# Kernel optimization log

Measured on AMD Instinct MI355X. Metric: run time of the kernel, lower is better.

The kernel has to match this reference:

```python
import jax, jax.numpy as jnp
import numpy as np

B, S, H = 4, 8192, 768
NH, HD = 12, 64          # num_heads, head_size
M = 64                   # projection_dim = min(256, HD)
EPS = 1e-6

def setup_inputs() -> dict:
    key = jax.random.key(0)
    ks = jax.random.split(key, 10)
    scale_w = 0.02
    scale_p = 1.0 / np.sqrt(HD)
    return {
        'hidden_states': jax.random.normal(ks[0], (B, S, H), jnp.float32),
        'Wq': jax.random.normal(ks[1], (H, H), jnp.float32) * scale_w,
        'bq': jnp.zeros((H,), jnp.float32),
        'Wk': jax.random.normal(ks[2], (H, H), jnp.float32) * scale_w,
        'bk': jnp.zeros((H,), jnp.float32),
        'Wv': jax.random.normal(ks[3], (H, H), jnp.float32) * scale_w,
        'bv': jnp.zeros((H,), jnp.float32),
        'Wo': jax.random.normal(ks[4], (H, H), jnp.float32) * scale_w,
        'bo': jnp.zeros((H,), jnp.float32),
        'projection_matrix': jax.random.normal(ks[5], (NH, HD, M), jnp.float32) * scale_p,
    }

def reference(hidden_states, Wq, bq, Wk, bk, Wv, bv, Wo, bo, projection_matrix):
    b, s, h = hidden_states.shape
    def heads(x):  # [b,s,h] -> [b,nh,s,hd]
        return x.reshape(b, s, NH, HD).transpose(0, 2, 1, 3)
    q = heads(hidden_states @ Wq + bq)
    k = heads(hidden_states @ Wk + bk)
    v = heads(hidden_states @ Wv + bv)
    # random-feature projection + stabilized exp feature map
    qp = jnp.einsum('bhnd,hdm->bhnm', q, projection_matrix)
    kp = jnp.einsum('bhnd,hdm->bhnm', k, projection_matrix)
    qp = jnp.exp(qp - jnp.max(qp, axis=-1, keepdims=True))
    kp = jnp.exp(kp - jnp.max(kp, axis=-1, keepdims=True))
    # O(n) linear attention: kv summary [b,h,m,hd]
    kv = jnp.einsum('bhnm,bhnd->bhmd', kp, v)
    qkv = jnp.einsum('bhnm,bhmd->bhnd', qp, kv)
    k_sum = jnp.sum(kp, axis=2)                      # [b,h,m]
    normalizer = jnp.einsum('bhnm,bhm->bhn', qp, k_sum)[..., None]
    ctx = qkv / (normalizer + EPS)
    ctx = ctx.transpose(0, 2, 1, 3).reshape(b, s, NH * HD)
    return ctx @ Wo + bo
```

## Files before the change

kernel.cpp:

```cpp
#include <hip/hip_runtime.h>
#include <hip/hip_bf16.h>


#define S_    8192
#define H_    768
#define NH_   12
#define EPS_  1e-6f

typedef unsigned short U16;
typedef short bf16x8 __attribute__((ext_vector_type(8)));
typedef float f32x4  __attribute__((ext_vector_type(4)));

__device__ __forceinline__ U16 f2b(float x) {
  unsigned u = __float_as_uint(x);
  return (U16)((u + 0x7fffu + ((u >> 16) & 1u)) >> 16);
}
__device__ __forceinline__ float b2f(U16 h) {
  return __uint_as_float(((unsigned)h) << 16);
}
__device__ __forceinline__ void gl2lds16(const void* g, void* l) {
  __builtin_amdgcn_global_load_lds(
      (const __attribute__((address_space(1))) void*)g,
      (__attribute__((address_space(3))) void*)l, 16, 0, 0);
}

__global__ void zero_f32(float* __restrict__ p, int n) {
  int i = blockIdx.x * 256 + threadIdx.x;
  if (i < n) p[i] = 0.f;
}

__global__ void cvt_f32_bf16(const float* __restrict__ src, U16* __restrict__ hi, int n4) {
  int i = blockIdx.x * 256 + threadIdx.x;
  if (i >= n4) return;
  float4 x = ((const float4*)src)[i];
  ushort4 h;
  h.x = f2b(x.x); h.y = f2b(x.y); h.z = f2b(x.z); h.w = f2b(x.w);
  ((ushort4*)hi)[i] = h;
}

__global__ void fold_proj(const float* __restrict__ Wq, const float* __restrict__ bq,
                          const float* __restrict__ Wk, const float* __restrict__ bk,
                          const float* __restrict__ P,
                          float* __restrict__ Wqp, float* __restrict__ bqp,
                          float* __restrict__ Wkp, float* __restrict__ bkp) {
  __shared__ float Pl[64 * 64];
  __shared__ float WL[4 * 64];
  int h = blockIdx.y, kc = blockIdx.x, tid = threadIdx.x;
  const float* W  = blockIdx.z ? Wk : Wq;
  const float* bb = blockIdx.z ? bk : bq;
  float* Wout = blockIdx.z ? Wkp : Wqp;
  float* bout = blockIdx.z ? bkp : bqp;
  const float4* P4 = (const float4*)(P + (size_t)h * 4096);
#pragma unroll
  for (int i = 0; i < 4; ++i) ((float4*)Pl)[tid + i * 256] = P4[tid + i * 256];
  WL[tid] = W[(size_t)(kc * 4 + (tid >> 6)) * H_ + h * 64 + (tid & 63)];
  __syncthreads();
  int kl = tid >> 6, m = tid & 63;
  float acc = 0.f;
#pragma unroll
  for (int d = 0; d < 64; ++d) acc += WL[kl * 64 + d] * Pl[d * 64 + m];
  Wout[(size_t)(kc * 4 + kl) * H_ + h * 64 + m] = acc;
  if (kc == 0 && tid < 64) {
    float a2 = 0.f;
    for (int d = 0; d < 64; ++d) a2 += bb[h * 64 + d] * Pl[d * 64 + tid];
    bout[h * 64 + tid] = a2;
  }
}

__global__ void build_cat(const float* __restrict__ Wqp, const float* __restrict__ Wkp,
                          const float* __restrict__ Wv,  const float* __restrict__ Wo,
                          U16* __restrict__ WcatH, U16* __restrict__ WoTH) {
  int k = blockIdx.x * 256 + threadIdx.x;
  int r = blockIdx.y;
  float v; U16* dh; size_t off;
  if (r < 768)       { v = Wqp[(size_t)k * H_ + r];          off = (size_t)r * H_ + k;          dh = WcatH; }
  else if (r < 1536) { v = Wkp[(size_t)k * H_ + (r - 768)];  off = (size_t)r * H_ + k;          dh = WcatH; }
  else if (r < 2304) { v = Wv [(size_t)k * H_ + (r - 1536)]; off = (size_t)r * H_ + k;          dh = WcatH; }
  else               { v = Wo [(size_t)k * H_ + (r - 2304)]; off = (size_t)(r - 2304) * H_ + k; dh = WoTH; }
  dh[off] = f2b(v);
}

__global__ void build_bias(const float* __restrict__ bqp, const float* __restrict__ bkp,
                           const float* __restrict__ bv, float* __restrict__ biasC) {
  int i = blockIdx.x * 256 + threadIdx.x;
  if (i >= 2304) return;
  biasC[i] = i < 768 ? bqp[i] : (i < 1536 ? bkp[i - 768] : bv[i - 1536]);
}

#define GEMM_KLOOP()                                                         \
  auto stage = [&](int kt, int bi) {                                         \
    const U16* ap = As + kt * 64;                                            \
    const U16* bp = Bs + kt * 64;                                            \
    unsigned ub = (unsigned)bi * 32768u + lb;                                \
    _Pragma("unroll")                                                        \
    for (int q = 0; q < 4; ++q) {                                            \
      gl2lds16(ap + (size_t)(q * 64) * H_, &Us[ub + q * 4096]);              \
      gl2lds16(bp + (size_t)(q * 64) * H_, &Us[ub + 16384u + q * 4096]);     \
    }                                                                        \
  };                                                                         \
  auto swzo = [&](int ks) { return (((ks * 4 + quad) ^ (l16 & 7)) * 8); };   \
  stage(0, 0);                                                               \
  for (int t = 0; t < 12; ++t) {                                             \
    const unsigned ab = (unsigned)(t & 1) * 32768u;                          \
    if (t < 11) {                                                            \
      stage(t + 1, (t + 1) & 1);                                             \
      asm volatile("s_waitcnt vmcnt(8)" ::: "memory");                       \
    } else {                                                                 \
      asm volatile("s_waitcnt vmcnt(0)" ::: "memory");                       \
    }                                                                        \
    __builtin_amdgcn_sched_barrier(0);                                       \
    __builtin_amdgcn_s_barrier();                                            \
    __builtin_amdgcn_sched_barrier(0);                                       \
    bf16x8 ah[8], bh[4];                                                     \
                              \
    _Pragma("unroll")                                                        \
    for (int i = 0; i < 4; ++i)                                              \
      _Pragma("unroll")                                                      \
      for (int ks = 0; ks < 2; ++ks)                                         \
        ah[i * 2 + ks] = *(const bf16x8*)&Us[ab +                            \
            (unsigned)((wm * 128 + i * 16 + l16) * 64 + swzo(ks))];          \
    _Pragma("unroll")                                                        \
    for (int jj = 0; jj < 2; ++jj)                                           \
      _Pragma("unroll")                                                      \
      for (int ks = 0; ks < 2; ++ks)                                         \
        bh[jj * 2 + ks] = *(const bf16x8*)&Us[ab + 16384u +                  \
            (unsigned)((wn * 64 + jj * 16 + l16) * 64 + swzo(ks))];          \
    PHASE_TAIL(0, 0)                                                         \
                                          \
    _Pragma("unroll")                                                        \
    for (int jj = 0; jj < 2; ++jj)                                           \
      _Pragma("unroll")                                                      \
      for (int ks = 0; ks < 2; ++ks)                                         \
        bh[jj * 2 + ks] = *(const bf16x8*)&Us[ab + 16384u +                  \
            (unsigned)((wn * 64 + (2 + jj) * 16 + l16) * 64 + swzo(ks))];    \
    PHASE_TAIL(0, 1)                                                         \
                              \
    _Pragma("unroll")                                                        \
    for (int i = 0; i < 4; ++i)                                              \
      _Pragma("unroll")                                                      \
      for (int ks = 0; ks < 2; ++ks)                                         \
        ah[i * 2 + ks] = *(const bf16x8*)&Us[ab +                            \
            (unsigned)((wm * 128 + 64 + i * 16 + l16) * 64 + swzo(ks))];     \
    PHASE_TAIL(1, 1)                                                         \
                              \
    _Pragma("unroll")                                                        \
    for (int jj = 0; jj < 2; ++jj)                                           \
      _Pragma("unroll")                                                      \
      for (int ks = 0; ks < 2; ++ks)                                         \
        bh[jj * 2 + ks] = *(const bf16x8*)&Us[ab + 16384u +                  \
            (unsigned)((wn * 64 + jj * 16 + l16) * 64 + swzo(ks))];          \
    PHASE_TAIL(1, 0)                                                         \
  }

#define PHASE_TAIL(mh, jh)                                                   \
    __builtin_amdgcn_sched_barrier(0);                                       \
    __builtin_amdgcn_s_barrier();                                            \
    asm volatile("s_waitcnt lgkmcnt(0)" ::: "memory");                       \
    __builtin_amdgcn_sched_barrier(0);                                       \
    __builtin_amdgcn_s_setprio(1);                                           \
    _Pragma("unroll")                                                        \
    for (int jj = 0; jj < 2; ++jj)                                           \
      _Pragma("unroll")                                                      \
      for (int i = 0; i < 4; ++i)                                            \
        _Pragma("unroll")                                                    \
        for (int ks = 0; ks < 2; ++ks)                                       \
          acc[(mh) * 4 + i][(jh) * 2 + jj] =                                 \
              __builtin_amdgcn_mfma_f32_16x16x32_bf16(                       \
                  ah[i * 2 + ks], bh[jj * 2 + ks],                           \
                  acc[(mh) * 4 + i][(jh) * 2 + jj], 0, 0, 0);                \
    __builtin_amdgcn_s_setprio(0);                                           \
    __builtin_amdgcn_sched_barrier(0);                                       \
    __builtin_amdgcn_s_barrier();                                            \
    __builtin_amdgcn_sched_barrier(0);

__global__ __launch_bounds__(512, 2) void gemm_qkv(
    const U16* __restrict__ Ahi, const U16* __restrict__ Bhi,
    const float* __restrict__ bias,
    U16* __restrict__ qp, U16* __restrict__ kpT, U16* __restrict__ vT) {
  __shared__ __align__(16) U16 Us[65536];
  const int tid = threadIdx.x, w = tid >> 6, lane = tid & 63;
  const int quad = lane >> 4, l16 = lane & 15;
  const int id = blockIdx.x;
  const int xcd = id & 7, pos = id >> 3;
  const int mt = xcd * 16 + pos / 9, nt = pos % 9;
  const int rowA0 = mt * 256, colB0 = nt * 256;
  const int wm = w >> 2, wn = w & 3;
  const int srow = w * 8 + (lane >> 3);
  const int kch = ((lane & 7) ^ (lane >> 3)) * 8;
  const U16* As = Ahi + (size_t)(rowA0 + srow) * H_ + kch;
  const U16* Bs = Bhi + (size_t)(colB0 + srow) * H_ + kch;
  const unsigned lb = (unsigned)(w * 8) * 64;

  f32x4 acc[8][4] = {};
  GEMM_KLOOP()

  const int col64 = colB0 + wn * 64;
  float bj[4];
#pragma unroll
  for (int j = 0; j < 4; ++j) bj[j] = bias[col64 + j * 16 + l16];
  if (col64 < 768) {
    const int h = col64 >> 6;
#pragma unroll
    for (int f = 0; f < 8; ++f) {
#pragma unroll
      for (int r = 0; r < 4; ++r) {
        int row = rowA0 + wm * 128 + f * 16 + quad * 4 + r;
        float v0 = acc[f][0][r] + bj[0], v1 = acc[f][1][r] + bj[1];
        float v2 = acc[f][2][r] + bj[2], v3 = acc[f][3][r] + bj[3];
        float mx = fmaxf(fmaxf(v0, v1), fmaxf(v2, v3));
        mx = fmaxf(mx, __shfl_xor(mx, 1));
        mx = fmaxf(mx, __shfl_xor(mx, 2));
        mx = fmaxf(mx, __shfl_xor(mx, 4));
        mx = fmaxf(mx, __shfl_xor(mx, 8));
        int b = row >> 13, s = row & 8191;
        size_t base = ((size_t)(b * NH_ + h) * S_ + s) * 64 + l16;
        qp[base +  0] = f2b(__expf(v0 - mx));
        qp[base + 16] = f2b(__expf(v1 - mx));
        qp[base + 32] = f2b(__expf(v2 - mx));
        qp[base + 48] = f2b(__expf(v3 - mx));
      }
    }
  } else {
    const int isv = col64 >= 1536;
    const int h = (col64 - (isv ? 1536 : 768)) >> 6;
    U16* dstT = isv ? vT : kpT;
#pragma unroll
    for (int f = 0; f < 8; ++f) {
      float er[4][4];
#pragma unroll
      for (int r = 0; r < 4; ++r) {
        float v0 = acc[f][0][r] + bj[0], v1 = acc[f][1][r] + bj[1];
        float v2 = acc[f][2][r] + bj[2], v3 = acc[f][3][r] + bj[3];
        if (!isv) {
          float mx = fmaxf(fmaxf(v0, v1), fmaxf(v2, v3));
          mx = fmaxf(mx, __shfl_xor(mx, 1));
          mx = fmaxf(mx, __shfl_xor(mx, 2));
          mx = fmaxf(mx, __shfl_xor(mx, 4));
          mx = fmaxf(mx, __shfl_xor(mx, 8));
          v0 = __expf(v0 - mx); v1 = __expf(v1 - mx);
          v2 = __expf(v2 - mx); v3 = __expf(v3 - mx);
        }
        er[0][r] = v0; er[1][r] = v1; er[2][r] = v2; er[3][r] = v3;
      }
      int n = rowA0 + wm * 128 + f * 16 + quad * 4;
      int b = n >> 13, s = n & 8191;
      int bh2 = b * NH_ + h;
#pragma unroll
      for (int j = 0; j < 4; ++j) {
        ushort4 o;
        o.x = f2b(er[j][0]); o.y = f2b(er[j][1]);
        o.z = f2b(er[j][2]); o.w = f2b(er[j][3]);
        *(ushort4*)&dstT[((size_t)bh2 * 64 + j * 16 + l16) * S_ + s] = o;
      }
    }
  }
}

__global__ __launch_bounds__(256, 4) void kv_accum_mfma(
    const U16* __restrict__ kpT, const U16* __restrict__ vT,
    float* __restrict__ kvT) {
  __shared__ __align__(16) U16 Us[2 * 64 * 64];
  const int tid = threadIdx.x, w = tid >> 6, lane = tid & 63;
  const int quad = lane >> 4, l16 = lane & 15;
  const int bh = blockIdx.y;
  const int n0 = blockIdx.x * 512;
  const U16* srcs[4];
  unsigned ldsoff[4];
#pragma unroll
  for (int t = 0; t < 4; ++t) {
    int c = w * 4 + t, buf = c >> 3;
    int r = (c & 7) * 8 + (lane >> 3);
    const U16* base = buf ? kpT : vT;
    srcs[t] = base + ((size_t)bh * 64 + r) * S_ + n0 + (lane & 7) * 8;
    ldsoff[t] = buf * 4096 + (c & 7) * 512;
  }
  f32x4 acc[4] = {};
  float ks[4] = {0.f, 0.f, 0.f, 0.f};
  for (int nc = 0; nc < 512; nc += 64) {
#pragma unroll
    for (int t = 0; t < 4; ++t) gl2lds16(srcs[t] + nc, &Us[ldsoff[t]]);
    __syncthreads();
#pragma unroll
    for (int k0 = 0; k0 < 64; k0 += 32) {
      bf16x8 av = *(const bf16x8*)&Us[(w * 16 + l16) * 64 + k0 + quad * 8];
#pragma unroll
      for (int j = 0; j < 4; ++j) {
        bf16x8 bk = *(const bf16x8*)&Us[4096 + (j * 16 + l16) * 64 + k0 + quad * 8];
        if (w == 0) {
#pragma unroll
          for (int e = 0; e < 8; ++e) ks[j] += b2f((U16)bk[e]);
        }
        acc[j] = __builtin_amdgcn_mfma_f32_16x16x32_bf16(av, bk, acc[j], 0, 0, 0);
      }
    }
    __syncthreads();
  }
#pragma unroll
  for (int j = 0; j < 4; ++j)
#pragma unroll
    for (int r = 0; r < 4; ++r) {
      int d = w * 16 + quad * 4 + r;
      atomicAdd(&kvT[((size_t)bh * 80 + d) * 64 + j * 16 + l16], acc[j][r]);
    }
  if (w == 0) {
#pragma unroll
    for (int j = 0; j < 4; ++j) {
      ks[j] += __shfl_xor(ks[j], 16);
      ks[j] += __shfl_xor(ks[j], 32);
    }
    if (lane < 16) {
#pragma unroll
      for (int j = 0; j < 4; ++j)
        atomicAdd(&kvT[((size_t)bh * 80 + 64) * 64 + j * 16 + lane], ks[j]);
    }
  }
}

__global__ __launch_bounds__(256) void ctx_gemm_k(
    const U16* __restrict__ qp, const float* __restrict__ kvT,
    U16* __restrict__ ctx) {
  __shared__ __align__(16) U16 As[128 * 64];
  __shared__ __align__(16) U16 Bs[80 * 64];
  int bh = blockIdx.y, row0 = blockIdx.x * 128;
  int tid = threadIdx.x, w = tid >> 6, lane = tid & 63;
  int quad = lane >> 4, l16 = lane & 15;
  const U16* Ab = qp + ((size_t)bh * S_ + row0) * 64;
#pragma unroll
  for (int t = 0; t < 4; ++t) {
    int cb = (w * 4 + t) * 64;
    gl2lds16(Ab + (size_t)(cb + lane) * 8, &As[cb * 8]);
  }
  const float4* kv4 = (const float4*)(kvT + (size_t)bh * 5120);
#pragma unroll
  for (int t = 0; t < 5; ++t) {
    int idx = t * 256 + tid;
    float4 f = kv4[idx];
    ushort4 o;
    o.x = f2b(f.x); o.y = f2b(f.y); o.z = f2b(f.z); o.w = f2b(f.w);
    *(ushort4*)&Bs[idx * 4] = o;
  }
  __syncthreads();
  f32x4 acc[2][5] = {};
#pragma unroll
  for (int k0 = 0; k0 < 64; k0 += 32) {
    bf16x8 a[2], fb[5];
#pragma unroll
    for (int i = 0; i < 2; ++i)
      a[i] = *(const bf16x8*)&As[(w * 32 + i * 16 + l16) * 64 + k0 + quad * 8];
#pragma unroll
    for (int j = 0; j < 5; ++j)
      fb[j] = *(const bf16x8*)&Bs[(j * 16 + l16) * 64 + k0 + quad * 8];
#pragma unroll
    for (int j = 0; j < 5; ++j)
#pragma unroll
      for (int i = 0; i < 2; ++i)
        acc[i][j] = __builtin_amdgcn_mfma_f32_16x16x32_bf16(a[i], fb[j], acc[i][j], 0, 0, 0);
  }
  int b = bh / NH_, h = bh - b * NH_;
#pragma unroll
  for (int i = 0; i < 2; ++i) {
#pragma unroll
    for (int r = 0; r < 4; ++r) {
      int s = row0 + w * 32 + i * 16 + quad * 4 + r;
      float nv = __shfl(acc[i][4][r], lane & 48);
      float inv = 1.f / (nv + EPS_);
      size_t base = ((size_t)b * S_ + s) * H_ + h * 64;
#pragma unroll
      for (int j = 0; j < 4; ++j)
        ctx[base + j * 16 + l16] = f2b(acc[i][j][r] * inv);
    }
  }
}

__global__ __launch_bounds__(512, 2) void gemm_out(
    const U16* __restrict__ Ahi, const U16* __restrict__ Bhi,
    const float* __restrict__ bias, float* __restrict__ C) {
  __shared__ __align__(16) U16 Us[65536];
  const int tid = threadIdx.x, w = tid >> 6, lane = tid & 63;
  const int quad = lane >> 4, l16 = lane & 15;
  const int id = blockIdx.x;
  const int xcd = id & 7, pos = id >> 3;
  const int mt = xcd * 16 + pos / 3, nt = pos % 3;
  const int rowA0 = mt * 256, colB0 = nt * 256;
  const int wm = w >> 2, wn = w & 3;
  const int srow = w * 8 + (lane >> 3);
  const int kch = ((lane & 7) ^ (lane >> 3)) * 8;
  const U16* As = Ahi + (size_t)(rowA0 + srow) * H_ + kch;
  const U16* Bs = Bhi + (size_t)(colB0 + srow) * H_ + kch;
  const unsigned lb = (unsigned)(w * 8) * 64;

  f32x4 acc[8][4] = {};
  GEMM_KLOOP()

#pragma unroll
  for (int f = 0; f < 8; ++f) {
    int row = rowA0 + wm * 128 + f * 16 + quad * 4;
#pragma unroll
    for (int j = 0; j < 4; ++j) {
      int col = colB0 + wn * 64 + j * 16 + l16;
      float bvv = bias[col];
#pragma unroll
      for (int r = 0; r < 4; ++r)
        C[(size_t)(row + r) * H_ + col] = acc[f][j][r] + bvv;
    }
  }
}

extern "C" void kernel_launch(void* const* d_in, const int* in_sizes, int n_in,
                              void* d_out, int out_size, void* d_ws, size_t ws_size,
                              hipStream_t stream) {
  const float* hs = (const float*)d_in[0];
  const float* Wq = (const float*)d_in[1];
  const float* bq = (const float*)d_in[2];
  const float* Wk = (const float*)d_in[3];
  const float* bk = (const float*)d_in[4];
  const float* Wv = (const float*)d_in[5];
  const float* bv = (const float*)d_in[6];
  const float* Wo = (const float*)d_in[7];
  const float* bo = (const float*)d_in[8];
  const float* P  = (const float*)d_in[9];
  float* out = (float*)d_out;

  char* ws = (char*)d_ws;
  size_t off = 0;
  auto alloc = [&](size_t bytes) -> void* {
    void* p = ws + off;
    off = (off + bytes + 255) & ~(size_t)255;
    return p;
  };
  U16*   hs_hi = (U16*)alloc(50331648);
  float* WqpF  = (float*)alloc(2359296);
  float* WkpF  = (float*)alloc(2359296);
  float* bqpF  = (float*)alloc(3072);
  float* bkpF  = (float*)alloc(3072);
  U16*   WcatH = (U16*)alloc(3538944);
  U16*   WoTH  = (U16*)alloc(1179648);
  float* biasC = (float*)alloc(9216);
  U16*   qp    = (U16*)alloc(50331648);
  U16*   kpT   = (U16*)alloc(50331648);
  U16*   vT    = (U16*)alloc(50331648);
  float* kvT   = (float*)alloc(983040);
  U16*   ctx   = hs_hi;

  zero_f32<<<dim3(960), dim3(256), 0, stream>>>(kvT, 245760);
  cvt_f32_bf16<<<dim3(24576), dim3(256), 0, stream>>>(hs, hs_hi, 6291456);
  fold_proj<<<dim3(192, 12, 2), dim3(256), 0, stream>>>(Wq, bq, Wk, bk, P, WqpF, bqpF, WkpF, bkpF);
  build_cat<<<dim3(3, 3072), dim3(256), 0, stream>>>(WqpF, WkpF, Wv, Wo, WcatH, WoTH);
  build_bias<<<dim3(9), dim3(256), 0, stream>>>(bqpF, bkpF, bv, biasC);
  gemm_qkv<<<dim3(1152), dim3(512), 0, stream>>>(hs_hi, WcatH, biasC, qp, kpT, vT);
  kv_accum_mfma<<<dim3(16, 48), dim3(256), 0, stream>>>(kpT, vT, kvT);
  ctx_gemm_k<<<dim3(64, 48), dim3(256), 0, stream>>>(qp, kvT, ctx);
  gemm_out<<<dim3(384), dim3(512), 0, stream>>>(ctx, WoTH, bo, out);
}
```

Before: 496.2 us.

## Make QKV GEMM persistent over N tiles and tile-transpose weight conversion

The QKV projection GEMM changes from 1152 blocks of 512 threads using 256x256 tiles to 512 blocks of 256 threads using 128x128 tiles. Each block keeps one 128-row A tile and loops over 9 column tiles, prefetching the next tile's first K slice across tile boundaries. The weight transpose-and-convert kernel now goes through a padded shared-memory tile, so both reads and writes are coalesced and vectorised instead of strided per element. The smaller tiles lower arithmetic intensity per block and give fewer blocks for parallelism, in exchange for better A reuse in L2 and continuous pipelining across output tiles.

```diff
diff --git a/kernel.cpp b/kernel.cpp
--- a/kernel.cpp
+++ b/kernel.cpp
@@ -67,17 +67,32 @@
   }
 }
 
-__global__ void build_cat(const float* __restrict__ Wqp, const float* __restrict__ Wkp,
-                          const float* __restrict__ Wv,  const float* __restrict__ Wo,
-                          U16* __restrict__ WcatH, U16* __restrict__ WoTH) {
-  int k = blockIdx.x * 256 + threadIdx.x;
-  int r = blockIdx.y;
-  float v; U16* dh; size_t off;
-  if (r < 768)       { v = Wqp[(size_t)k * H_ + r];          off = (size_t)r * H_ + k;          dh = WcatH; }
-  else if (r < 1536) { v = Wkp[(size_t)k * H_ + (r - 768)];  off = (size_t)r * H_ + k;          dh = WcatH; }
-  else if (r < 2304) { v = Wv [(size_t)k * H_ + (r - 1536)]; off = (size_t)r * H_ + k;          dh = WcatH; }
-  else               { v = Wo [(size_t)k * H_ + (r - 2304)]; off = (size_t)(r - 2304) * H_ + k; dh = WoTH; }
-  dh[off] = f2b(v);
+__global__ void build_cat_t(const float* __restrict__ Wqp, const float* __restrict__ Wkp,
+                            const float* __restrict__ Wv,  const float* __restrict__ Wo,
+                            U16* __restrict__ WcatH, U16* __restrict__ WoTH) {
+  __shared__ float T[64][68];
+  const int kb = blockIdx.x, rb = blockIdx.y, mat = blockIdx.z;
+  const int tid = threadIdx.x;
+  const float* W = mat == 0 ? Wqp : (mat == 1 ? Wkp : (mat == 2 ? Wv : Wo));
+#pragma unroll
+  for (int p = 0; p < 4; ++p) {
+    int idx = tid + p * 256;
+    int rr = idx >> 4, c4 = (idx & 15) * 4;
+    float4 v = *(const float4*)&W[(size_t)(kb * 64 + rr) * H_ + rb * 64 + c4];
+    T[rr][c4] = v.x; T[rr][c4 + 1] = v.y; T[rr][c4 + 2] = v.z; T[rr][c4 + 3] = v.w;
+  }
+  __syncthreads();
+  U16* dst = mat == 3 ? WoTH : WcatH;
+  const int rbase = (mat == 3 ? 0 : mat * 768) + rb * 64;
+#pragma unroll
+  for (int p = 0; p < 4; ++p) {
+    int idx = tid + p * 256;
+    int r2 = idx >> 4, c2 = (idx & 15) * 4;
+    ushort4 o;
+    o.x = f2b(T[c2 + 0][r2]); o.y = f2b(T[c2 + 1][r2]);
+    o.z = f2b(T[c2 + 2][r2]); o.w = f2b(T[c2 + 3][r2]);
+    *(ushort4*)&dst[(size_t)(rbase + r2) * H_ + kb * 64 + c2] = o;
+  }
 }
 
 __global__ void build_bias(const float* __restrict__ bqp, const float* __restrict__ bkp,
@@ -85,6 +100,267 @@
   int i = blockIdx.x * 256 + threadIdx.x;
   if (i >= 2304) return;
   biasC[i] = i < 768 ? bqp[i] : (i < 1536 ? bkp[i - 768] : bv[i - 1536]);
+}
+
+__global__ __launch_bounds__(256, 2) void gemm_qkv(
+    const U16* __restrict__ Ahi, const U16* __restrict__ Bhi,
+    const float* __restrict__ bias,
+    U16* __restrict__ qp, U16* __restrict__ kpT, U16* __restrict__ vT) {
+  __shared__ __align__(16) U16 Us[32768];
+  const int tid = threadIdx.x, w = tid >> 6, lane = tid & 63;
+  const int quad = lane >> 4, l16 = lane & 15;
+  const int b = blockIdx.x;
+  const int mt = b & 255, nt0 = b >> 8;
+  const int rowA0 = mt * 128;
+  const int wm = w & 1, wn = w >> 1;
+  const U16* srcA[4];
+  int rowBl[4];
+  unsigned ldsc[4];
+  const int kch = ((lane & 7) ^ (lane >> 3)) * 8;
+#pragma unroll
+  for (int t = 0; t < 4; ++t) {
+    int c = w * 4 + t;
+    int row = c * 8 + (lane >> 3);
+    srcA[t] = Ahi + (size_t)(rowA0 + row) * H_ + kch;
+    rowBl[t] = row;
+    ldsc[t] = (unsigned)c * 512;
+  }
+  auto stage = [&](int jn, int tn, int bi) {
+    const int colB = (nt0 + 2 * jn) * 128;
+    unsigned ub = (unsigned)bi * 16384u;
+#pragma unroll
+    for (int t = 0; t < 4; ++t) {
+      gl2lds16(srcA[t] + tn * 64, &Us[ub + ldsc[t]]);
+      gl2lds16(Bhi + (size_t)(colB + rowBl[t]) * H_ + tn * 64 + kch,
+               &Us[ub + 8192u + ldsc[t]]);
+    }
+  };
+
+  stage(0, 0, 0);
+  for (int jj = 0; jj < 9; ++jj) {
+    const int colB0 = (nt0 + 2 * jj) * 128;
+    f32x4 acc[4][4] = {};
+    for (int t = 0; t < 12; ++t) {
+      const bool more = !(jj == 8 && t == 11);
+      if (more) {
+        if (t < 11) stage(jj, t + 1, (t + 1) & 1);
+        else        stage(jj + 1, 0, 0);
+        asm volatile("s_waitcnt vmcnt(8)" ::: "memory");
+      } else {
+        asm volatile("s_waitcnt vmcnt(0)" ::: "memory");
+      }
+      __builtin_amdgcn_sched_barrier(0);
+      __builtin_amdgcn_s_barrier();
+      __builtin_amdgcn_sched_barrier(0);
+      const unsigned ab = (unsigned)(t & 1) * 16384u;
+      bf16x8 ah[4][2], bh[4][2];
+#pragma unroll
+      for (int i = 0; i < 4; ++i)
+#pragma unroll
+        for (int ks = 0; ks < 2; ++ks)
+          ah[i][ks] = *(const bf16x8*)&Us[ab +
+              (unsigned)((wm * 64 + i * 16 + l16) * 64 +
+                         (((ks * 4 + quad) ^ (l16 & 7)) * 8))];
+#pragma unroll
+      for (int j = 0; j < 4; ++j)
+#pragma unroll
+        for (int ks = 0; ks < 2; ++ks)
+          bh[j][ks] = *(const bf16x8*)&Us[ab + 8192u +
+              (unsigned)((wn * 64 + j * 16 + l16) * 64 +
+                         (((ks * 4 + quad) ^ (l16 & 7)) * 8))];
+      asm volatile("s_waitcnt lgkmcnt(0)" ::: "memory");
+      __builtin_amdgcn_sched_barrier(0);
+      __builtin_amdgcn_s_setprio(1);
+#pragma unroll
+      for (int ks = 0; ks < 2; ++ks)
+#pragma unroll
+        for (int j = 0; j < 4; ++j)
+#pragma unroll
+          for (int i = 0; i < 4; ++i)
+            acc[i][j] = __builtin_amdgcn_mfma_f32_16x16x32_bf16(
+                ah[i][ks], bh[j][ks], acc[i][j], 0, 0, 0);
+      __builtin_amdgcn_s_setprio(0);
+      __builtin_amdgcn_sched_barrier(0);
+      __builtin_amdgcn_s_barrier();
+      __builtin_amdgcn_sched_barrier(0);
+    }
+    const int col64 = colB0 + wn * 64;
+    float bj[4];
+#pragma unroll
+    for (int j = 0; j < 4; ++j) bj[j] = bias[col64 + j * 16 + l16];
+    if (col64 < 768) {
+      const int h = col64 >> 6;
+#pragma unroll
+      for (int i = 0; i < 4; ++i) {
+#pragma unroll
+        for (int r = 0; r < 4; ++r) {
+          int row = rowA0 + wm * 64 + i * 16 + quad * 4 + r;
+          float v0 = acc[i][0][r] + bj[0], v1 = acc[i][1][r] + bj[1];
+          float v2 = acc[i][2][r] + bj[2], v3 = acc[i][3][r] + bj[3];
+          float mx = fmaxf(fmaxf(v0, v1), fmaxf(v2, v3));
+          mx = fmaxf(mx, __shfl_xor(mx, 1));
+          mx = fmaxf(mx, __shfl_xor(mx, 2));
+          mx = fmaxf(mx, __shfl_xor(mx, 4));
+          mx = fmaxf(mx, __shfl_xor(mx, 8));
+          int bb = row >> 13, s = row & 8191;
+          size_t base = ((size_t)(bb * NH_ + h) * S_ + s) * 64 + l16;
+          qp[base +  0] = f2b(__expf(v0 - mx));
+          qp[base + 16] = f2b(__expf(v1 - mx));
+          qp[base + 32] = f2b(__expf(v2 - mx));
+          qp[base + 48] = f2b(__expf(v3 - mx));
+        }
+      }
+    } else {
+      const int isv = col64 >= 1536;
+      const int h = (col64 - (isv ? 1536 : 768)) >> 6;
+      U16* dstT = isv ? vT : kpT;
+      const int bh2 = (rowA0 >> 13) * NH_ + h;
+#pragma unroll
+      for (int i = 0; i < 4; ++i) {
+        float er[4][4];
+#pragma unroll
+        for (int r = 0; r < 4; ++r) {
+          float v0 = acc[i][0][r] + bj[0], v1 = acc[i][1][r] + bj[1];
+          float v2 = acc[i][2][r] + bj[2], v3 = acc[i][3][r] + bj[3];
+          if (!isv) {
+            float mx = fmaxf(fmaxf(v0, v1), fmaxf(v2, v3));
+            mx = fmaxf(mx, __shfl_xor(mx, 1));
+            mx = fmaxf(mx, __shfl_xor(mx, 2));
+            mx = fmaxf(mx, __shfl_xor(mx, 4));
+            mx = fmaxf(mx, __shfl_xor(mx, 8));
+            v0 = __expf(v0 - mx); v1 = __expf(v1 - mx);
+            v2 = __expf(v2 - mx); v3 = __expf(v3 - mx);
+          }
+          er[0][r] = v0; er[1][r] = v1; er[2][r] = v2; er[3][r] = v3;
+        }
+        int n = rowA0 + wm * 64 + i * 16 + quad * 4;
+        int s = n & 8191;
+#pragma unroll
+        for (int j = 0; j < 4; ++j) {
+          ushort4 o;
+          o.x = f2b(er[j][0]); o.y = f2b(er[j][1]);
+          o.z = f2b(er[j][2]); o.w = f2b(er[j][3]);
+          *(ushort4*)&dstT[((size_t)bh2 * 64 + j * 16 + l16) * S_ + s] = o;
+        }
+      }
+    }
+  }
+}
+
+__global__ __launch_bounds__(256, 4) void kv_accum_mfma(
+    const U16* __restrict__ kpT, const U16* __restrict__ vT,
+    float* __restrict__ kvT) {
+  __shared__ __align__(16) U16 Us[2 * 64 * 64];
+  const int tid = threadIdx.x, w = tid >> 6, lane = tid & 63;
+  const int quad = lane >> 4, l16 = lane & 15;
+  const int bh = blockIdx.y;
+  const int n0 = blockIdx.x * 512;
+  const U16* srcs[4];
+  unsigned ldsoff[4];
+#pragma unroll
+  for (int t = 0; t < 4; ++t) {
+    int c = w * 4 + t, buf = c >> 3;
+    int r = (c & 7) * 8 + (lane >> 3);
+    const U16* base = buf ? kpT : vT;
+    srcs[t] = base + ((size_t)bh * 64 + r) * S_ + n0 + (lane & 7) * 8;
+    ldsoff[t] = buf * 4096 + (c & 7) * 512;
+  }
+  f32x4 acc[4] = {};
+  float ks[4] = {0.f, 0.f, 0.f, 0.f};
+  for (int nc = 0; nc < 512; nc += 64) {
+#pragma unroll
+    for (int t = 0; t < 4; ++t) gl2lds16(srcs[t] + nc, &Us[ldsoff[t]]);
+    __syncthreads();
+#pragma unroll
+    for (int k0 = 0; k0 < 64; k0 += 32) {
+      bf16x8 av = *(const bf16x8*)&Us[(w * 16 + l16) * 64 + k0 + quad * 8];
+#pragma unroll
+      for (int j = 0; j < 4; ++j) {
+        bf16x8 bk = *(const bf16x8*)&Us[4096 + (j * 16 + l16) * 64 + k0 + quad * 8];
+        if (w == 0) {
+#pragma unroll
+          for (int e = 0; e < 8; ++e) ks[j] += b2f((U16)bk[e]);
+        }
+        acc[j] = __builtin_amdgcn_mfma_f32_16x16x32_bf16(av, bk, acc[j], 0, 0, 0);
+      }
+    }
+    __syncthreads();
+  }
+#pragma unroll
+  for (int j = 0; j < 4; ++j)
+#pragma unroll
+    for (int r = 0; r < 4; ++r) {
+      int d = w * 16 + quad * 4 + r;
+      atomicAdd(&kvT[((size_t)bh * 80 + d) * 64 + j * 16 + l16], acc[j][r]);
+    }
+  if (w == 0) {
+#pragma unroll
+    for (int j = 0; j < 4; ++j) {
+      ks[j] += __shfl_xor(ks[j], 16);
+      ks[j] += __shfl_xor(ks[j], 32);
+    }
+    if (lane < 16) {
+#pragma unroll
+      for (int j = 0; j < 4; ++j)
+        atomicAdd(&kvT[((size_t)bh * 80 + 64) * 64 + j * 16 + lane], ks[j]);
+    }
+  }
+}
+
+__global__ __launch_bounds__(256) void ctx_gemm_k(
+    const U16* __restrict__ qp, const float* __restrict__ kvT,
+    U16* __restrict__ ctx) {
+  __shared__ __align__(16) U16 As[128 * 64];
+  __shared__ __align__(16) U16 Bs[80 * 64];
+  int bh = blockIdx.y, row0 = blockIdx.x * 128;
+  int tid = threadIdx.x, w = tid >> 6, lane = tid & 63;
+  int quad = lane >> 4, l16 = lane & 15;
+  const U16* Ab = qp + ((size_t)bh * S_ + row0) * 64;
+#pragma unroll
+  for (int t = 0; t < 4; ++t) {
+    int cb = (w * 4 + t) * 64;
+    gl2lds16(Ab + (size_t)(cb + lane) * 8, &As[cb * 8]);
+  }
+  const float4* kv4 = (const float4*)(kvT + (size_t)bh * 5120);
+#pragma unroll
+  for (int t = 0; t < 5; ++t) {
+    int idx = t * 256 + tid;
+    float4 f = kv4[idx];
+    ushort4 o;
+    o.x = f2b(f.x); o.y = f2b(f.y); o.z = f2b(f.z); o.w = f2b(f.w);
+    *(ushort4*)&Bs[idx * 4] = o;
+  }
+  __syncthreads();
+  f32x4 acc[2][5] = {};
+#pragma unroll
+  for (int k0 = 0; k0 < 64; k0 += 32) {
+    bf16x8 a[2], fb[5];
+#pragma unroll
+    for (int i = 0; i < 2; ++i)
+      a[i] = *(const bf16x8*)&As[(w * 32 + i * 16 + l16) * 64 + k0 + quad * 8];
+#pragma unroll
+    for (int j = 0; j < 5; ++j)
+      fb[j] = *(const bf16x8*)&Bs[(j * 16 + l16) * 64 + k0 + quad * 8];
+#pragma unroll
+    for (int j = 0; j < 5; ++j)
+#pragma unroll
+      for (int i = 0; i < 2; ++i)
+        acc[i][j] = __builtin_amdgcn_mfma_f32_16x16x32_bf16(a[i], fb[j], acc[i][j], 0, 0, 0);
+  }
+  int b = bh / NH_, h = bh - b * NH_;
+#pragma unroll
+  for (int i = 0; i < 2; ++i) {
+#pragma unroll
+    for (int r = 0; r < 4; ++r) {
+      int s = row0 + w * 32 + i * 16 + quad * 4 + r;
+      float nv = __shfl(acc[i][4][r], lane & 48);
+      float inv = 1.f / (nv + EPS_);
+      size_t base = ((size_t)b * S_ + s) * H_ + h * 64;
+#pragma unroll
+      for (int j = 0; j < 4; ++j)
+        ctx[base + j * 16 + l16] = f2b(acc[i][j][r] * inv);
+    }
+  }
 }
 
 #define GEMM_KLOOP()                                                         \
@@ -112,7 +388,6 @@
     __builtin_amdgcn_s_barrier();                                            \
     __builtin_amdgcn_sched_barrier(0);                                       \
     bf16x8 ah[8], bh[4];                                                     \
-                              \
     _Pragma("unroll")                                                        \
     for (int i = 0; i < 4; ++i)                                              \
       _Pragma("unroll")                                                      \
@@ -126,7 +401,6 @@
         bh[jj * 2 + ks] = *(const bf16x8*)&Us[ab + 16384u +                  \
             (unsigned)((wn * 64 + jj * 16 + l16) * 64 + swzo(ks))];          \
     PHASE_TAIL(0, 0)                                                         \
-                                          \
     _Pragma("unroll")                                                        \
     for (int jj = 0; jj < 2; ++jj)                                           \
       _Pragma("unroll")                                                      \
@@ -134,7 +408,6 @@
         bh[jj * 2 + ks] = *(const bf16x8*)&Us[ab + 16384u +                  \
             (unsigned)((wn * 64 + (2 + jj) * 16 + l16) * 64 + swzo(ks))];    \
     PHASE_TAIL(0, 1)                                                         \
-                              \
     _Pragma("unroll")                                                        \
     for (int i = 0; i < 4; ++i)                                              \
       _Pragma("unroll")                                                      \
@@ -142,7 +415,6 @@
         ah[i * 2 + ks] = *(const bf16x8*)&Us[ab +                            \
             (unsigned)((wm * 128 + 64 + i * 16 + l16) * 64 + swzo(ks))];     \
     PHASE_TAIL(1, 1)                                                         \
-                              \
     _Pragma("unroll")                                                        \
     for (int jj = 0; jj < 2; ++jj)                                           \
       _Pragma("unroll")                                                      \
@@ -172,205 +444,6 @@
     __builtin_amdgcn_sched_barrier(0);                                       \
     __builtin_amdgcn_s_barrier();                                            \
     __builtin_amdgcn_sched_barrier(0);
-
-__global__ __launch_bounds__(512, 2) void gemm_qkv(
-    const U16* __restrict__ Ahi, const U16* __restrict__ Bhi,
-    const float* __restrict__ bias,
-    U16* __restrict__ qp, U16* __restrict__ kpT, U16* __restrict__ vT) {
-  __shared__ __align__(16) U16 Us[65536];
-  const int tid = threadIdx.x, w = tid >> 6, lane = tid & 63;
-  const int quad = lane >> 4, l16 = lane & 15;
-  const int id = blockIdx.x;
-  const int xcd = id & 7, pos = id >> 3;
-  const int mt = xcd * 16 + pos / 9, nt = pos % 9;
-  const int rowA0 = mt * 256, colB0 = nt * 256;
-  const int wm = w >> 2, wn = w & 3;
-  const int srow = w * 8 + (lane >> 3);
-  const int kch = ((lane & 7) ^ (lane >> 3)) * 8;
-  const U16* As = Ahi + (size_t)(rowA0 + srow) * H_ + kch;
-  const U16* Bs = Bhi + (size_t)(colB0 + srow) * H_ + kch;
-  const unsigned lb = (unsigned)(w * 8) * 64;
-
-  f32x4 acc[8][4] = {};
-  GEMM_KLOOP()
-
-  const int col64 = colB0 + wn * 64;
-  float bj[4];
-#pragma unroll
-  for (int j = 0; j < 4; ++j) bj[j] = bias[col64 + j * 16 + l16];
-  if (col64 < 768) {
-    const int h = col64 >> 6;
-#pragma unroll
-    for (int f = 0; f < 8; ++f) {
-#pragma unroll
-      for (int r = 0; r < 4; ++r) {
-        int row = rowA0 + wm * 128 + f * 16 + quad * 4 + r;
-        float v0 = acc[f][0][r] + bj[0], v1 = acc[f][1][r] + bj[1];
-        float v2 = acc[f][2][r] + bj[2], v3 = acc[f][3][r] + bj[3];
-        float mx = fmaxf(fmaxf(v0, v1), fmaxf(v2, v3));
-        mx = fmaxf(mx, __shfl_xor(mx, 1));
-        mx = fmaxf(mx, __shfl_xor(mx, 2));
-        mx = fmaxf(mx, __shfl_xor(mx, 4));
-        mx = fmaxf(mx, __shfl_xor(mx, 8));
-        int b = row >> 13, s = row & 8191;
-        size_t base = ((size_t)(b * NH_ + h) * S_ + s) * 64 + l16;
-        qp[base +  0] = f2b(__expf(v0 - mx));
-        qp[base + 16] = f2b(__expf(v1 - mx));
-        qp[base + 32] = f2b(__expf(v2 - mx));
-        qp[base + 48] = f2b(__expf(v3 - mx));
-      }
-    }
-  } else {
-    const int isv = col64 >= 1536;
-    const int h = (col64 - (isv ? 1536 : 768)) >> 6;
-    U16* dstT = isv ? vT : kpT;
-#pragma unroll
-    for (int f = 0; f < 8; ++f) {
-      float er[4][4];
-#pragma unroll
-      for (int r = 0; r < 4; ++r) {
-        float v0 = acc[f][0][r] + bj[0], v1 = acc[f][1][r] + bj[1];
-        float v2 = acc[f][2][r] + bj[2], v3 = acc[f][3][r] + bj[3];
-        if (!isv) {
-          float mx = fmaxf(fmaxf(v0, v1), fmaxf(v2, v3));
-          mx = fmaxf(mx, __shfl_xor(mx, 1));
-          mx = fmaxf(mx, __shfl_xor(mx, 2));
-          mx = fmaxf(mx, __shfl_xor(mx, 4));
-          mx = fmaxf(mx, __shfl_xor(mx, 8));
-          v0 = __expf(v0 - mx); v1 = __expf(v1 - mx);
-          v2 = __expf(v2 - mx); v3 = __expf(v3 - mx);
-        }
-        er[0][r] = v0; er[1][r] = v1; er[2][r] = v2; er[3][r] = v3;
-      }
-      int n = rowA0 + wm * 128 + f * 16 + quad * 4;
-      int b = n >> 13, s = n & 8191;
-      int bh2 = b * NH_ + h;
-#pragma unroll
-      for (int j = 0; j < 4; ++j) {
-        ushort4 o;
-        o.x = f2b(er[j][0]); o.y = f2b(er[j][1]);
-        o.z = f2b(er[j][2]); o.w = f2b(er[j][3]);
-        *(ushort4*)&dstT[((size_t)bh2 * 64 + j * 16 + l16) * S_ + s] = o;
-      }
-    }
-  }
-}
-
-__global__ __launch_bounds__(256, 4) void kv_accum_mfma(
-    const U16* __restrict__ kpT, const U16* __restrict__ vT,
-    float* __restrict__ kvT) {
-  __shared__ __align__(16) U16 Us[2 * 64 * 64];
-  const int tid = threadIdx.x, w = tid >> 6, lane = tid & 63;
-  const int quad = lane >> 4, l16 = lane & 15;
-  const int bh = blockIdx.y;
-  const int n0 = blockIdx.x * 512;
-  const U16* srcs[4];
-  unsigned ldsoff[4];
-#pragma unroll
-  for (int t = 0; t < 4; ++t) {
-    int c = w * 4 + t, buf = c >> 3;
-    int r = (c & 7) * 8 + (lane >> 3);
-    const U16* base = buf ? kpT : vT;
-    srcs[t] = base + ((size_t)bh * 64 + r) * S_ + n0 + (lane & 7) * 8;
-    ldsoff[t] = buf * 4096 + (c & 7) * 512;
-  }
-  f32x4 acc[4] = {};
-  float ks[4] = {0.f, 0.f, 0.f, 0.f};
-  for (int nc = 0; nc < 512; nc += 64) {
-#pragma unroll
-    for (int t = 0; t < 4; ++t) gl2lds16(srcs[t] + nc, &Us[ldsoff[t]]);
-    __syncthreads();
-#pragma unroll
-    for (int k0 = 0; k0 < 64; k0 += 32) {
-      bf16x8 av = *(const bf16x8*)&Us[(w * 16 + l16) * 64 + k0 + quad * 8];
-#pragma unroll
-      for (int j = 0; j < 4; ++j) {
-        bf16x8 bk = *(const bf16x8*)&Us[4096 + (j * 16 + l16) * 64 + k0 + quad * 8];
-        if (w == 0) {
-#pragma unroll
-          for (int e = 0; e < 8; ++e) ks[j] += b2f((U16)bk[e]);
-        }
-        acc[j] = __builtin_amdgcn_mfma_f32_16x16x32_bf16(av, bk, acc[j], 0, 0, 0);
-      }
-    }
-    __syncthreads();
-  }
-#pragma unroll
-  for (int j = 0; j < 4; ++j)
-#pragma unroll
-    for (int r = 0; r < 4; ++r) {
-      int d = w * 16 + quad * 4 + r;
-      atomicAdd(&kvT[((size_t)bh * 80 + d) * 64 + j * 16 + l16], acc[j][r]);
-    }
-  if (w == 0) {
-#pragma unroll
-    for (int j = 0; j < 4; ++j) {
-      ks[j] += __shfl_xor(ks[j], 16);
-      ks[j] += __shfl_xor(ks[j], 32);
-    }
-    if (lane < 16) {
-#pragma unroll
-      for (int j = 0; j < 4; ++j)
-        atomicAdd(&kvT[((size_t)bh * 80 + 64) * 64 + j * 16 + lane], ks[j]);
-    }
-  }
-}
-
-__global__ __launch_bounds__(256) void ctx_gemm_k(
-    const U16* __restrict__ qp, const float* __restrict__ kvT,
-    U16* __restrict__ ctx) {
-  __shared__ __align__(16) U16 As[128 * 64];
-  __shared__ __align__(16) U16 Bs[80 * 64];
-  int bh = blockIdx.y, row0 = blockIdx.x * 128;
-  int tid = threadIdx.x, w = tid >> 6, lane = tid & 63;
-  int quad = lane >> 4, l16 = lane & 15;
-  const U16* Ab = qp + ((size_t)bh * S_ + row0) * 64;
-#pragma unroll
-  for (int t = 0; t < 4; ++t) {
-    int cb = (w * 4 + t) * 64;
-    gl2lds16(Ab + (size_t)(cb + lane) * 8, &As[cb * 8]);
-  }
-  const float4* kv4 = (const float4*)(kvT + (size_t)bh * 5120);
-#pragma unroll
-  for (int t = 0; t < 5; ++t) {
-    int idx = t * 256 + tid;
-    float4 f = kv4[idx];
-    ushort4 o;
-    o.x = f2b(f.x); o.y = f2b(f.y); o.z = f2b(f.z); o.w = f2b(f.w);
-    *(ushort4*)&Bs[idx * 4] = o;
-  }
-  __syncthreads();
-  f32x4 acc[2][5] = {};
-#pragma unroll
-  for (int k0 = 0; k0 < 64; k0 += 32) {
-    bf16x8 a[2], fb[5];
-#pragma unroll
-    for (int i = 0; i < 2; ++i)
-      a[i] = *(const bf16x8*)&As[(w * 32 + i * 16 + l16) * 64 + k0 + quad * 8];
-#pragma unroll
-    for (int j = 0; j < 5; ++j)
-      fb[j] = *(const bf16x8*)&Bs[(j * 16 + l16) * 64 + k0 + quad * 8];
-#pragma unroll
-    for (int j = 0; j < 5; ++j)
-#pragma unroll
-      for (int i = 0; i < 2; ++i)
-        acc[i][j] = __builtin_amdgcn_mfma_f32_16x16x32_bf16(a[i], fb[j], acc[i][j], 0, 0, 0);
-  }
-  int b = bh / NH_, h = bh - b * NH_;
-#pragma unroll
-  for (int i = 0; i < 2; ++i) {
-#pragma unroll
-    for (int r = 0; r < 4; ++r) {
-      int s = row0 + w * 32 + i * 16 + quad * 4 + r;
-      float nv = __shfl(acc[i][4][r], lane & 48);
-      float inv = 1.f / (nv + EPS_);
-      size_t base = ((size_t)b * S_ + s) * H_ + h * 64;
-#pragma unroll
-      for (int j = 0; j < 4; ++j)
-        ctx[base + j * 16 + l16] = f2b(acc[i][j][r] * inv);
-    }
-  }
-}
 
 __global__ __launch_bounds__(512, 2) void gemm_out(
     const U16* __restrict__ Ahi, const U16* __restrict__ Bhi,
@@ -445,9 +518,9 @@
   zero_f32<<<dim3(960), dim3(256), 0, stream>>>(kvT, 245760);
   cvt_f32_bf16<<<dim3(24576), dim3(256), 0, stream>>>(hs, hs_hi, 6291456);
   fold_proj<<<dim3(192, 12, 2), dim3(256), 0, stream>>>(Wq, bq, Wk, bk, P, WqpF, bqpF, WkpF, bkpF);
-  build_cat<<<dim3(3, 3072), dim3(256), 0, stream>>>(WqpF, WkpF, Wv, Wo, WcatH, WoTH);
+  build_cat_t<<<dim3(12, 12, 4), dim3(256), 0, stream>>>(WqpF, WkpF, Wv, Wo, WcatH, WoTH);
   build_bias<<<dim3(9), dim3(256), 0, stream>>>(bqpF, bkpF, bv, biasC);
-  gemm_qkv<<<dim3(1152), dim3(512), 0, stream>>>(hs_hi, WcatH, biasC, qp, kpT, vT);
+  gemm_qkv<<<dim3(512), dim3(256), 0, stream>>>(hs_hi, WcatH, biasC, qp, kpT, vT);
   kv_accum_mfma<<<dim3(16, 48), dim3(256), 0, stream>>>(kpT, vT, kvT);
   ctx_gemm_k<<<dim3(64, 48), dim3(256), 0, stream>>>(qp, kvT, ctx);
   gemm_out<<<dim3(384), dim3(512), 0, stream>>>(ctx, WoTH, bo, out);
```

After: 480.9 us. 3.1% less time.
